# Kernel tuning notes

Measured on AMD Instinct MI355X. Metric: run time of the kernel, lower is better.

## Reference

```python
import jax, jax.numpy as jnp
import numpy as np

PREFIX = 20000
LEAF = 50000
NONLEAF = 50000
NUMD = 8 * NONLEAF  # 400000 fine-depth nodes
C = 256


def setup_inputs() -> dict:
    key = jax.random.key(0)
    k1, k2 = jax.random.split(key)
    n_rows = PREFIX + LEAF + NUMD
    x = jax.random.normal(k1, (n_rows, C), dtype=jnp.float32)
    # xavier-uniform-like init for Downsample weights (C_out, C_in, 8)
    limit = float(np.sqrt(6.0 / (C + C * 8)))
    weights = jax.random.uniform(k2, (C, C, 8), dtype=jnp.float32,
                                 minval=-limit, maxval=limit)
    # children at depth-1: alternate leaf (-1) / non-leaf (+1) -> exactly LEAF leaves
    children = jnp.where(jnp.arange(LEAF + NONLEAF) % 2 == 0, -1, 1).astype(jnp.int32)
    return {"x": x, "weights": weights, "children": children,
            "numd": NUMD, "leaf_num": LEAF}


def reference(x, weights, children, numd, leaf_num):
    c = x.shape[1]
    # Downsample: groups of 8 fine nodes -> one coarse node.
    # torch: x.view(-1, 8*C) @ weights.flatten(1).t()
    outd = x[-numd:].reshape(-1, 8 * c) @ weights.reshape(c, 8 * c).T  # [numd/8, C]

    leaf_mask = children < 0                      # [nnum_prev]
    lm = leaf_mask.astype(jnp.int32)
    rank_leaf = jnp.cumsum(lm) - lm               # rank among leaf positions
    nlm = 1 - lm
    rank_nonleaf = jnp.cumsum(nlm) - nlm          # rank among non-leaf positions
    # out[leaf_mask] = x[-leaf_num-numd:-numd]; out[~leaf_mask] = outd
    idx = jnp.where(leaf_mask, rank_leaf, leaf_num + rank_nonleaf)
    x_leaf = x[-(leaf_num + numd):-numd]          # [leaf_num, C]
    combined = jnp.concatenate([x_leaf, outd], axis=0)
    merged = combined[idx]                        # [nnum_prev, C]

    prefix = x.shape[0] - leaf_num - numd
    return jnp.concatenate([x[:prefix], merged], axis=0)
```

## Files before the change

### kernel.cpp

```cpp
#include <hip/hip_runtime.h>
#include <hip/hip_bf16.h>

#define PREFIX_N 20000
#define LEAF_N   50000
#define NONLEAF_N 50000
#define CH_N     (LEAF_N + NONLEAF_N)
#define CCOL     256
#define GK       2048
#define GM       NONLEAF_N
#define OUT_ROWS (PREFIX_N + CH_N)
#define NKT      (GK / 32)

typedef float  f32x4v __attribute__((ext_vector_type(4)));
typedef __bf16 bf16x8 __attribute__((ext_vector_type(8)));
typedef short  s16x8  __attribute__((ext_vector_type(8)));

static __device__ __forceinline__ unsigned pk2(float a, float b) {
  __hip_bfloat16 ha = __float2bfloat16(a);
  __hip_bfloat16 hb = __float2bfloat16(b);
  unsigned short sa = __builtin_bit_cast(unsigned short, ha);
  unsigned short sb = __builtin_bit_cast(unsigned short, hb);
  return (unsigned)sa | ((unsigned)sb << 16);
}
static __device__ __forceinline__ uint4 pack8(const float4& x, const float4& y) {
  uint4 r;
  r.x = pk2(x.x, x.y); r.y = pk2(x.z, x.w);
  r.z = pk2(y.x, y.y); r.w = pk2(y.z, y.w);
  return r;
}

__global__ __launch_bounds__(256) void count_leaves(const int* __restrict__ ch,
                                                    int n, int* __restrict__ cnt) {
  int gi = blockIdx.x * 256 + threadIdx.x;
  int lm = (gi < n && ch[gi] < 0) ? 1 : 0;
  unsigned long long mask = __ballot(lm);
  __shared__ int wsum[4];
  int lane = threadIdx.x & 63, w = threadIdx.x >> 6;
  if (lane == 0) wsum[w] = __popcll(mask);
  __syncthreads();
  if (threadIdx.x == 0) cnt[blockIdx.x] = wsum[0] + wsum[1] + wsum[2] + wsum[3];
}

__global__ __launch_bounds__(512) void scan_blocks(const int* __restrict__ cnt,
                                                   int* __restrict__ boff, int nb) {
  __shared__ int s[512];
  int t = threadIdx.x;
  int v = (t < nb) ? cnt[t] : 0;
  s[t] = v;
  __syncthreads();
  for (int d = 1; d < 512; d <<= 1) {
    int add = (t >= d) ? s[t - d] : 0;
    __syncthreads();
    s[t] += add;
    __syncthreads();
  }
  if (t < nb) boff[t] = s[t] - v;
}

__global__ __launch_bounds__(256) void rank_kernel(const int* __restrict__ ch,
                                                   const int* __restrict__ boff, int n,
                                                   int* __restrict__ idx,
                                                   int* __restrict__ rowof) {
  int gi = blockIdx.x * 256 + threadIdx.x;
  int lane = threadIdx.x & 63, w = threadIdx.x >> 6;
  int lm = (gi < n && ch[gi] < 0) ? 1 : 0;
  unsigned long long mask = __ballot(lm);
  int lrank = __popcll(mask & ((1ull << lane) - 1ull));
  __shared__ int wcnt[4];
  if (lane == 63) wcnt[w] = lrank + lm;
  __syncthreads();
  int woff = 0;
  for (int i = 0; i < w; ++i) woff += wcnt[i];
  if (gi < n) {
    int rl = boff[blockIdx.x] + woff + lrank;
    if (lm) {
      idx[gi] = rl;
    } else {
      int rn = gi - rl;
      idx[gi] = LEAF_N + rn;
      rowof[rn] = gi;
    }
  }
}

__global__ __launch_bounds__(256) void copy_rows(const float* __restrict__ x,
                                                 const int* __restrict__ idx,
                                                 float* __restrict__ out) {
  int row = blockIdx.x * 4 + (threadIdx.x >> 6);
  if (row >= OUT_ROWS) return;
  int lane = threadIdx.x & 63;
  const float* src;
  if (row < PREFIX_N) {
    src = x + (size_t)row * CCOL;
  } else {
    int id = idx[row - PREFIX_N];
    if (id >= LEAF_N) return;
    src = x + (size_t)(PREFIX_N + id) * CCOL;
  }
  float4 v = ((const float4*)src)[lane];
  ((float4*)(out + (size_t)row * CCOL))[lane] = v;
}

__global__ __launch_bounds__(512, 2) void gemm_kernel(const float* __restrict__ A,
                                                      const float* __restrict__ W,
                                                      const int* __restrict__ rowof,
                                                      float* __restrict__ out) {
  __shared__ unsigned short Alds[128][40];
  __shared__ unsigned short Blds[256][40];
  __shared__ int tgt[128];

  const int tid  = threadIdx.x;
  const int lane = tid & 63;
  const int w    = tid >> 6;
  const int wm   = w >> 2;
  const int wn   = w & 3;
  const int tile_m = blockIdx.x;

  if (tid < 128) {
    int m = tile_m * 128 + tid;
    tgt[tid] = (m < GM) ? (PREFIX_N + rowof[m]) : -1;
  }

  const int ar = tid >> 2;
  const int ac = (tid & 3) * 8;
  const int br = tid >> 1;
  const int bc = (tid & 1) * 16;

  int agr = tile_m * 128 + ar;
  if (agr >= GM) agr = GM - 1;
  const float* aptr = A + (size_t)agr * GK + ac;
  const float* bptr = W + (size_t)br  * GK + bc;

  f32x4v acc[4][4] = {};

  float4 fa0, fa1, fb0, fb1, fb2, fb3;
  fa0 = ((const float4*)aptr)[0]; fa1 = ((const float4*)aptr)[1];
  fb0 = ((const float4*)bptr)[0]; fb1 = ((const float4*)bptr)[1];
  fb2 = ((const float4*)bptr)[2]; fb3 = ((const float4*)bptr)[3];
  uint4 aS  = pack8(fa0, fa1);
  uint4 bS0 = pack8(fb0, fb1);
  uint4 bS1 = pack8(fb2, fb3);

  const int lr = lane & 15, lq = lane >> 4;

  for (int kt = 0; kt < NKT; ++kt) {
    __syncthreads();
    *(uint4*)&Alds[ar][ac]     = aS;
    *(uint4*)&Blds[br][bc]     = bS0;
    *(uint4*)&Blds[br][bc + 8] = bS1;
    __syncthreads();

    if (kt + 1 < NKT) {
      const float* ap = aptr + (kt + 1) * 32;
      fa0 = ((const float4*)ap)[0]; fa1 = ((const float4*)ap)[1];
      const float* bp = bptr + (kt + 1) * 32;
      fb0 = ((const float4*)bp)[0]; fb1 = ((const float4*)bp)[1];
      fb2 = ((const float4*)bp)[2]; fb3 = ((const float4*)bp)[3];
    }

    s16x8 af[4], bf[4];
#pragma unroll
    for (int fm = 0; fm < 4; ++fm)
      af[fm] = *(const s16x8*)&Alds[wm * 64 + fm * 16 + lr][lq * 8];
#pragma unroll
    for (int fn = 0; fn < 4; ++fn)
      bf[fn] = *(const s16x8*)&Blds[wn * 64 + fn * 16 + lr][lq * 8];
#pragma unroll
    for (int fm = 0; fm < 4; ++fm)
#pragma unroll
      for (int fn = 0; fn < 4; ++fn)
        acc[fm][fn] = __builtin_amdgcn_mfma_f32_16x16x32_bf16(
            __builtin_bit_cast(bf16x8, af[fm]),
            __builtin_bit_cast(bf16x8, bf[fn]),
            acc[fm][fn], 0, 0, 0);

    if (kt + 1 < NKT) {
      aS  = pack8(fa0, fa1);
      bS0 = pack8(fb0, fb1);
      bS1 = pack8(fb2, fb3);
    }
  }

#pragma unroll
  for (int fm = 0; fm < 4; ++fm) {
    int mlb = wm * 64 + fm * 16 + lq * 4;
    int t0 = tgt[mlb + 0], t1 = tgt[mlb + 1], t2 = tgt[mlb + 2], t3 = tgt[mlb + 3];
#pragma unroll
    for (int fn = 0; fn < 4; ++fn) {
      int col = wn * 64 + fn * 16 + lr;
      if (t0 >= 0) out[(size_t)t0 * CCOL + col] = acc[fm][fn][0];
      if (t1 >= 0) out[(size_t)t1 * CCOL + col] = acc[fm][fn][1];
      if (t2 >= 0) out[(size_t)t2 * CCOL + col] = acc[fm][fn][2];
      if (t3 >= 0) out[(size_t)t3 * CCOL + col] = acc[fm][fn][3];
    }
  }
}

extern "C" void kernel_launch(void* const* d_in, const int* in_sizes, int n_in,
                              void* d_out, int out_size, void* d_ws, size_t ws_size,
                              hipStream_t stream) {
  const float* x        = (const float*)d_in[0];
  const float* wts      = (const float*)d_in[1];
  const int*   children = (const int*)d_in[2];
  float*       out      = (float*)d_out;

  int* wsp   = (int*)d_ws;
  int* cnt   = wsp;
  int* boff  = wsp + 512;
  int* idx   = wsp + 1024;
  int* rowof = wsp + 1024 + CH_N;

  const int nb = (CH_N + 255) / 256;

  count_leaves<<<nb, 256, 0, stream>>>(children, CH_N, cnt);
  scan_blocks<<<1, 512, 0, stream>>>(cnt, boff, nb);
  rank_kernel<<<nb, 256, 0, stream>>>(children, boff, CH_N, idx, rowof);

  copy_rows<<<(OUT_ROWS + 3) / 4, 256, 0, stream>>>(x, idx, out);

  const float* A = x + (size_t)(PREFIX_N + LEAF_N) * CCOL;
  gemm_kernel<<<(GM + 127) / 128, 512, 0, stream>>>(A, wts, rowof, out);
}
```

Baseline: 204.1 us.

## Pre-convert weights to bf16 and double-buffer GEMM tiles with direct global-to-LDS loads

A new kernel converts the weights to bf16 once per call into workspace. The GEMM then streams B tiles straight into LDS with global_load_lds, using XOR-swizzled, double-buffered LDS tiles for both operands. A tiles are prefetched two k-steps ahead in registers. This removes per-block fp32-to-bf16 conversion of W and overlaps loads with MFMA work, at the cost of an extra launch, more LDS, hand-placed waitcnt/barrier sequencing and dropping the occupancy hint of 2.

```diff
diff --git a/kernel.cpp b/kernel.cpp
--- a/kernel.cpp
+++ b/kernel.cpp
@@ -27,6 +27,18 @@
   r.x = pk2(x.x, x.y); r.y = pk2(x.z, x.w);
   r.z = pk2(y.x, y.y); r.w = pk2(y.z, y.w);
   return r;
+}
+
+#define GLDS16(g, l) __builtin_amdgcn_global_load_lds(                      \
+    (const __attribute__((address_space(1))) void*)(g),                     \
+    (__attribute__((address_space(3))) void*)(l), 16, 0, 0)
+
+__global__ __launch_bounds__(256) void wcvt(const float* __restrict__ W,
+                                            unsigned short* __restrict__ Wb) {
+  int i = blockIdx.x * 256 + threadIdx.x;
+  float4 a = ((const float4*)W)[i * 2];
+  float4 b = ((const float4*)W)[i * 2 + 1];
+  *(uint4*)&Wb[i * 8] = pack8(a, b);
 }
 
 __global__ __launch_bounds__(256) void count_leaves(const int* __restrict__ ch,
@@ -101,12 +113,12 @@
   ((float4*)(out + (size_t)row * CCOL))[lane] = v;
 }
 
-__global__ __launch_bounds__(512, 2) void gemm_kernel(const float* __restrict__ A,
-                                                      const float* __restrict__ W,
-                                                      const int* __restrict__ rowof,
-                                                      float* __restrict__ out) {
-  __shared__ unsigned short Alds[128][40];
-  __shared__ unsigned short Blds[256][40];
+__global__ __launch_bounds__(512) void gemm_kernel(const float* __restrict__ A,
+                                                   const unsigned short* __restrict__ Wb,
+                                                   const int* __restrict__ rowof,
+                                                   float* __restrict__ out) {
+  __shared__ unsigned short Abuf[2][128 * 32];
+  __shared__ unsigned short Bbuf[2][256 * 32];
   __shared__ int tgt[128];
 
   const int tid  = threadIdx.x;
@@ -114,6 +126,7 @@
   const int w    = tid >> 6;
   const int wm   = w >> 2;
   const int wn   = w & 3;
+  const int lr   = lane & 15, lq = lane >> 4;
   const int tile_m = blockIdx.x;
 
   if (tid < 128) {
@@ -123,63 +136,77 @@
 
   const int ar = tid >> 2;
   const int ac = (tid & 3) * 8;
-  const int br = tid >> 1;
-  const int bc = (tid & 1) * 16;
-
   int agr = tile_m * 128 + ar;
   if (agr >= GM) agr = GM - 1;
   const float* aptr = A + (size_t)agr * GK + ac;
-  const float* bptr = W + (size_t)br  * GK + bc;
+  const int awidx = ar * 32 + (((tid & 3) ^ ((ar >> 1) & 3)) << 3);
+
+  const int brow0 = (w << 4) + (lane >> 2);
+  const int bch0  = (lane & 3) ^ ((brow0 >> 1) & 3);
+  const int brow1 = brow0 + 128;
+  const int bch1  = (lane & 3) ^ ((brow1 >> 1) & 3);
+  const char* bsrc0 = (const char*)Wb + (size_t)brow0 * (GK * 2) + (bch0 << 4);
+  const char* bsrc1 = (const char*)Wb + (size_t)brow1 * (GK * 2) + (bch1 << 4);
+  char* bd0_0 = (char*)&Bbuf[0][0] + tid * 16;
+  char* bd1_0 = bd0_0 + 8192;
+  char* bd0_1 = (char*)&Bbuf[1][0] + tid * 16;
+  char* bd1_1 = bd0_1 + 8192;
+
+  int aidx[4], bidx[4];
+#pragma unroll
+  for (int fm = 0; fm < 4; ++fm) {
+    int row = wm * 64 + fm * 16 + lr;
+    aidx[fm] = row * 32 + ((lq ^ ((row >> 1) & 3)) << 3);
+  }
+#pragma unroll
+  for (int fn = 0; fn < 4; ++fn) {
+    int row = wn * 64 + fn * 16 + lr;
+    bidx[fn] = row * 32 + ((lq ^ ((row >> 1) & 3)) << 3);
+  }
 
   f32x4v acc[4][4] = {};
-
-  float4 fa0, fa1, fb0, fb1, fb2, fb3;
-  fa0 = ((const float4*)aptr)[0]; fa1 = ((const float4*)aptr)[1];
-  fb0 = ((const float4*)bptr)[0]; fb1 = ((const float4*)bptr)[1];
-  fb2 = ((const float4*)bptr)[2]; fb3 = ((const float4*)bptr)[3];
-  uint4 aS  = pack8(fa0, fa1);
-  uint4 bS0 = pack8(fb0, fb1);
-  uint4 bS1 = pack8(fb2, fb3);
-
-  const int lr = lane & 15, lq = lane >> 4;
-
-  for (int kt = 0; kt < NKT; ++kt) {
-    __syncthreads();
-    *(uint4*)&Alds[ar][ac]     = aS;
-    *(uint4*)&Blds[br][bc]     = bS0;
-    *(uint4*)&Blds[br][bc + 8] = bS1;
-    __syncthreads();
-
-    if (kt + 1 < NKT) {
-      const float* ap = aptr + (kt + 1) * 32;
-      fa0 = ((const float4*)ap)[0]; fa1 = ((const float4*)ap)[1];
-      const float* bp = bptr + (kt + 1) * 32;
-      fb0 = ((const float4*)bp)[0]; fb1 = ((const float4*)bp)[1];
-      fb2 = ((const float4*)bp)[2]; fb3 = ((const float4*)bp)[3];
-    }
-
-    s16x8 af[4], bf[4];
-#pragma unroll
-    for (int fm = 0; fm < 4; ++fm)
-      af[fm] = *(const s16x8*)&Alds[wm * 64 + fm * 16 + lr][lq * 8];
-#pragma unroll
-    for (int fn = 0; fn < 4; ++fn)
-      bf[fn] = *(const s16x8*)&Blds[wn * 64 + fn * 16 + lr][lq * 8];
-#pragma unroll
-    for (int fm = 0; fm < 4; ++fm)
-#pragma unroll
-      for (int fn = 0; fn < 4; ++fn)
-        acc[fm][fn] = __builtin_amdgcn_mfma_f32_16x16x32_bf16(
-            __builtin_bit_cast(bf16x8, af[fm]),
-            __builtin_bit_cast(bf16x8, bf[fn]),
-            acc[fm][fn], 0, 0, 0);
-
-    if (kt + 1 < NKT) {
-      aS  = pack8(fa0, fa1);
-      bS0 = pack8(fb0, fb1);
-      bS1 = pack8(fb2, fb3);
-    }
-  }
+  float4 rAa0, rAa1, rAb0, rAb1;
+
+  GLDS16(bsrc0, bd0_0); GLDS16(bsrc1, bd1_0);
+  rAa0 = ((const float4*)aptr)[0]; rAa1 = ((const float4*)aptr)[1];
+  GLDS16(bsrc0 + 64, bd0_1); GLDS16(bsrc1 + 64, bd1_1);
+  rAb0 = ((const float4*)(aptr + 32))[0]; rAb1 = ((const float4*)(aptr + 32))[1];
+  *(uint4*)&Abuf[0][awidx] = pack8(rAa0, rAa1);
+  asm volatile("s_waitcnt lgkmcnt(0)" ::: "memory");
+  __builtin_amdgcn_s_barrier();
+
+#define GBODY(n_, CUR, RAc0, RAc1, RAl0, RAl1, BD0, BD1)                     \
+  {                                                                          \
+    s16x8 af[4], bf[4];                                                      \
+    _Pragma("unroll") for (int fm = 0; fm < 4; ++fm)                         \
+        af[fm] = *(const s16x8*)&Abuf[CUR][aidx[fm]];                        \
+    _Pragma("unroll") for (int fn = 0; fn < 4; ++fn)                         \
+        bf[fn] = *(const s16x8*)&Bbuf[CUR][bidx[fn]];                        \
+    asm volatile("s_waitcnt lgkmcnt(0)" ::: "memory");                       \
+    __builtin_amdgcn_s_barrier();                                            \
+    if ((n_) + 1 < NKT)                                                      \
+      *(uint4*)&Abuf[CUR ^ 1][awidx] = pack8(RAc0, RAc1);                    \
+    if ((n_) + 2 < NKT) {                                                    \
+      GLDS16(bsrc0 + ((n_) + 2) * 64, BD0);                                  \
+      GLDS16(bsrc1 + ((n_) + 2) * 64, BD1);                                  \
+      RAl0 = ((const float4*)(aptr + ((n_) + 2) * 32))[0];                   \
+      RAl1 = ((const float4*)(aptr + ((n_) + 2) * 32))[1];                   \
+    }                                                                        \
+    _Pragma("unroll") for (int fm = 0; fm < 4; ++fm)                         \
+      _Pragma("unroll") for (int fn = 0; fn < 4; ++fn)                       \
+          acc[fm][fn] = __builtin_amdgcn_mfma_f32_16x16x32_bf16(             \
+              __builtin_bit_cast(bf16x8, af[fm]),                            \
+              __builtin_bit_cast(bf16x8, bf[fn]), acc[fm][fn], 0, 0, 0);     \
+    asm volatile("s_waitcnt lgkmcnt(0)" ::: "memory");                       \
+    __builtin_amdgcn_s_barrier();                                            \
+  }
+
+#pragma unroll 1
+  for (int n = 0; n < NKT; n += 2) {
+    GBODY(n,     0, rAb0, rAb1, rAa0, rAa1, bd0_0, bd1_0);
+    GBODY(n + 1, 1, rAa0, rAa1, rAb0, rAb1, bd0_1, bd1_1);
+  }
+#undef GBODY
 
 #pragma unroll
   for (int fm = 0; fm < 4; ++fm) {
@@ -209,9 +236,11 @@
   int* boff  = wsp + 512;
   int* idx   = wsp + 1024;
   int* rowof = wsp + 1024 + CH_N;
+  unsigned short* Wb = (unsigned short*)((char*)d_ws + (1 << 20));
 
   const int nb = (CH_N + 255) / 256;
 
+  wcvt<<<256, 256, 0, stream>>>(wts, Wb);
   count_leaves<<<nb, 256, 0, stream>>>(children, CH_N, cnt);
   scan_blocks<<<1, 512, 0, stream>>>(cnt, boff, nb);
   rank_kernel<<<nb, 256, 0, stream>>>(children, boff, CH_N, idx, rowof);
@@ -219,5 +248,5 @@
   copy_rows<<<(OUT_ROWS + 3) / 4, 256, 0, stream>>>(x, idx, out);
 
   const float* A = x + (size_t)(PREFIX_N + LEAF_N) * CCOL;
-  gemm_kernel<<<(GM + 127) / 128, 512, 0, stream>>>(A, wts, rowof, out);
-}
+  gemm_kernel<<<(GM + 127) / 128, 512, 0, stream>>>(A, Wb, rowof, out);
+}
```

Result: slower. 224.3 us (+9.9%).

## Pre-convert weights to bf16, fuse row copy into GEMM, stream B from global

Applied to the files above, without the earlier changes.

The weight matrix is converted to bf16 once in a prep kernel that also counts leaves. The GEMM now uses 64-row tiles, 256 threads and double-buffered A in LDS with a K-step of 64, and B fragments are read directly from the bf16 global copy, leaving LDS for A only. The leaf and prefix row copy is folded into the same launch as extra blocks using a scatter map (leafof), which removes a kernel launch and the idx array. The intent is to cut weight conversion work, launch count and LDS traffic. In exchange, B reloads from global/L2 per tile become heavier and there are more GEMM blocks.

```diff
diff --git a/kernel.cpp b/kernel.cpp
--- a/kernel.cpp
+++ b/kernel.cpp
@@ -9,7 +9,12 @@
 #define GK       2048
 #define GM       NONLEAF_N
 #define OUT_ROWS (PREFIX_N + CH_N)
-#define NKT      (GK / 32)
+#define BM       64
+#define BKT      64
+#define NKT      (GK / BKT)
+#define TILES    ((GM + BM - 1) / BM)
+#define COPYROWS (PREFIX_N + LEAF_N)
+#define COPYBLK  ((COPYROWS + 3) / 4)
 
 typedef float  f32x4v __attribute__((ext_vector_type(4)));
 typedef __bf16 bf16x8 __attribute__((ext_vector_type(8)));
@@ -29,16 +34,26 @@
   return r;
 }
 
-__global__ __launch_bounds__(256) void count_leaves(const int* __restrict__ ch,
-                                                    int n, int* __restrict__ cnt) {
-  int gi = blockIdx.x * 256 + threadIdx.x;
-  int lm = (gi < n && ch[gi] < 0) ? 1 : 0;
-  unsigned long long mask = __ballot(lm);
-  __shared__ int wsum[4];
-  int lane = threadIdx.x & 63, w = threadIdx.x >> 6;
-  if (lane == 0) wsum[w] = __popcll(mask);
-  __syncthreads();
-  if (threadIdx.x == 0) cnt[blockIdx.x] = wsum[0] + wsum[1] + wsum[2] + wsum[3];
+__global__ __launch_bounds__(256) void prep_kernel(const float* __restrict__ W,
+                                                   unsigned short* __restrict__ Wb,
+                                                   const int* __restrict__ ch,
+                                                   int* __restrict__ cnt) {
+  if (blockIdx.x < 256) {
+    int i = blockIdx.x * 256 + threadIdx.x;
+    float4 a = ((const float4*)W)[i * 2];
+    float4 b = ((const float4*)W)[i * 2 + 1];
+    *(uint4*)&Wb[i * 8] = pack8(a, b);
+  } else {
+    int blk = blockIdx.x - 256;
+    int gi = blk * 256 + threadIdx.x;
+    int lm = (gi < CH_N && ch[gi] < 0) ? 1 : 0;
+    unsigned long long mask = __ballot(lm);
+    __shared__ int wsum[4];
+    int lane = threadIdx.x & 63, w = threadIdx.x >> 6;
+    if (lane == 0) wsum[w] = __popcll(mask);
+    __syncthreads();
+    if (threadIdx.x == 0) cnt[blk] = wsum[0] + wsum[1] + wsum[2] + wsum[3];
+  }
 }
 
 __global__ __launch_bounds__(512) void scan_blocks(const int* __restrict__ cnt,
@@ -59,8 +74,8 @@
 
 __global__ __launch_bounds__(256) void rank_kernel(const int* __restrict__ ch,
                                                    const int* __restrict__ boff, int n,
-                                                   int* __restrict__ idx,
-                                                   int* __restrict__ rowof) {
+                                                   int* __restrict__ rowof,
+                                                   int* __restrict__ leafof) {
   int gi = blockIdx.x * 256 + threadIdx.x;
   int lane = threadIdx.x & 63, w = threadIdx.x >> 6;
   int lm = (gi < n && ch[gi] < 0) ? 1 : 0;
@@ -73,117 +88,108 @@
   for (int i = 0; i < w; ++i) woff += wcnt[i];
   if (gi < n) {
     int rl = boff[blockIdx.x] + woff + lrank;
-    if (lm) {
-      idx[gi] = rl;
-    } else {
-      int rn = gi - rl;
-      idx[gi] = LEAF_N + rn;
-      rowof[rn] = gi;
-    }
-  }
-}
-
-__global__ __launch_bounds__(256) void copy_rows(const float* __restrict__ x,
-                                                 const int* __restrict__ idx,
-                                                 float* __restrict__ out) {
-  int row = blockIdx.x * 4 + (threadIdx.x >> 6);
-  if (row >= OUT_ROWS) return;
-  int lane = threadIdx.x & 63;
-  const float* src;
-  if (row < PREFIX_N) {
-    src = x + (size_t)row * CCOL;
-  } else {
-    int id = idx[row - PREFIX_N];
-    if (id >= LEAF_N) return;
-    src = x + (size_t)(PREFIX_N + id) * CCOL;
-  }
-  float4 v = ((const float4*)src)[lane];
-  ((float4*)(out + (size_t)row * CCOL))[lane] = v;
-}
-
-__global__ __launch_bounds__(512, 2) void gemm_kernel(const float* __restrict__ A,
-                                                      const float* __restrict__ W,
+    if (lm) leafof[rl] = gi;
+    else    rowof[gi - rl] = gi;
+  }
+}
+
+__global__ __launch_bounds__(256, 3) void main_kernel(const float* __restrict__ x,
+                                                      const float* __restrict__ A,
+                                                      const unsigned short* __restrict__ Wb,
                                                       const int* __restrict__ rowof,
+                                                      const int* __restrict__ leafof,
                                                       float* __restrict__ out) {
-  __shared__ unsigned short Alds[128][40];
-  __shared__ unsigned short Blds[256][40];
-  __shared__ int tgt[128];
+  __shared__ unsigned short Al[2][BM * 72];
+  __shared__ int tgt[BM];
 
   const int tid  = threadIdx.x;
   const int lane = tid & 63;
-  const int w    = tid >> 6;
-  const int wm   = w >> 2;
-  const int wn   = w & 3;
-  const int tile_m = blockIdx.x;
-
-  if (tid < 128) {
-    int m = tile_m * 128 + tid;
+
+  if (blockIdx.x >= TILES) {
+    int j = (blockIdx.x - TILES) * 4 + (tid >> 6);
+    if (j >= COPYROWS) return;
+    const float* src;
+    float* dst;
+    if (j < PREFIX_N) {
+      src = x + (size_t)j * CCOL;
+      dst = out + (size_t)j * CCOL;
+    } else {
+      int r = j - PREFIX_N;
+      src = x + (size_t)(PREFIX_N + r) * CCOL;
+      dst = out + (size_t)(PREFIX_N + leafof[r]) * CCOL;
+    }
+    ((float4*)dst)[lane] = ((const float4*)src)[lane];
+    return;
+  }
+
+  const int wn = tid >> 6;
+  const int lr = lane & 15, lq = lane >> 4;
+  const int tile = blockIdx.x;
+
+  if (tid < BM) {
+    int m = tile * BM + tid;
     tgt[tid] = (m < GM) ? (PREFIX_N + rowof[m]) : -1;
   }
 
   const int ar = tid >> 2;
-  const int ac = (tid & 3) * 8;
-  const int br = tid >> 1;
-  const int bc = (tid & 1) * 16;
-
-  int agr = tile_m * 128 + ar;
+  const int ac = (tid & 3) * 16;
+  int agr = tile * BM + ar;
   if (agr >= GM) agr = GM - 1;
   const float* aptr = A + (size_t)agr * GK + ac;
-  const float* bptr = W + (size_t)br  * GK + bc;
+  const int aw = ar * 72 + ac;
+
+  const unsigned short* bbase[4];
+#pragma unroll
+  for (int fn = 0; fn < 4; ++fn)
+    bbase[fn] = Wb + (size_t)(wn * 64 + fn * 16 + lr) * GK + lq * 8;
+
+  int aidx[4];
+#pragma unroll
+  for (int fm = 0; fm < 4; ++fm)
+    aidx[fm] = (fm * 16 + lr) * 72 + lq * 8;
 
   f32x4v acc[4][4] = {};
-
-  float4 fa0, fa1, fb0, fb1, fb2, fb3;
-  fa0 = ((const float4*)aptr)[0]; fa1 = ((const float4*)aptr)[1];
-  fb0 = ((const float4*)bptr)[0]; fb1 = ((const float4*)bptr)[1];
-  fb2 = ((const float4*)bptr)[2]; fb3 = ((const float4*)bptr)[3];
-  uint4 aS  = pack8(fa0, fa1);
-  uint4 bS0 = pack8(fb0, fb1);
-  uint4 bS1 = pack8(fb2, fb3);
-
-  const int lr = lane & 15, lq = lane >> 4;
-
+  float4 r0, r1, r2, r3;
+  r0 = ((const float4*)aptr)[0]; r1 = ((const float4*)aptr)[1];
+  r2 = ((const float4*)aptr)[2]; r3 = ((const float4*)aptr)[3];
+
+  int cur = 0;
+#pragma unroll 1
   for (int kt = 0; kt < NKT; ++kt) {
-    __syncthreads();
-    *(uint4*)&Alds[ar][ac]     = aS;
-    *(uint4*)&Blds[br][bc]     = bS0;
-    *(uint4*)&Blds[br][bc + 8] = bS1;
+    *(uint4*)&Al[cur][aw]     = pack8(r0, r1);
+    *(uint4*)&Al[cur][aw + 8] = pack8(r2, r3);
     __syncthreads();
 
     if (kt + 1 < NKT) {
-      const float* ap = aptr + (kt + 1) * 32;
-      fa0 = ((const float4*)ap)[0]; fa1 = ((const float4*)ap)[1];
-      const float* bp = bptr + (kt + 1) * 32;
-      fb0 = ((const float4*)bp)[0]; fb1 = ((const float4*)bp)[1];
-      fb2 = ((const float4*)bp)[2]; fb3 = ((const float4*)bp)[3];
-    }
-
-    s16x8 af[4], bf[4];
-#pragma unroll
-    for (int fm = 0; fm < 4; ++fm)
-      af[fm] = *(const s16x8*)&Alds[wm * 64 + fm * 16 + lr][lq * 8];
-#pragma unroll
-    for (int fn = 0; fn < 4; ++fn)
-      bf[fn] = *(const s16x8*)&Blds[wn * 64 + fn * 16 + lr][lq * 8];
-#pragma unroll
-    for (int fm = 0; fm < 4; ++fm)
+      const float* p = aptr + (kt + 1) * BKT;
+      r0 = ((const float4*)p)[0]; r1 = ((const float4*)p)[1];
+      r2 = ((const float4*)p)[2]; r3 = ((const float4*)p)[3];
+    }
+
+#pragma unroll
+    for (int ks = 0; ks < 2; ++ks) {
+      s16x8 af[4], bf[4];
+#pragma unroll
+      for (int fm = 0; fm < 4; ++fm)
+        af[fm] = *(const s16x8*)&Al[cur][aidx[fm] + ks * 32];
 #pragma unroll
       for (int fn = 0; fn < 4; ++fn)
-        acc[fm][fn] = __builtin_amdgcn_mfma_f32_16x16x32_bf16(
-            __builtin_bit_cast(bf16x8, af[fm]),
-            __builtin_bit_cast(bf16x8, bf[fn]),
-            acc[fm][fn], 0, 0, 0);
-
-    if (kt + 1 < NKT) {
-      aS  = pack8(fa0, fa1);
-      bS0 = pack8(fb0, fb1);
-      bS1 = pack8(fb2, fb3);
-    }
+        bf[fn] = *(const s16x8*)&bbase[fn][kt * BKT + ks * 32];
+#pragma unroll
+      for (int fm = 0; fm < 4; ++fm)
+#pragma unroll
+        for (int fn = 0; fn < 4; ++fn)
+          acc[fm][fn] = __builtin_amdgcn_mfma_f32_16x16x32_bf16(
+              __builtin_bit_cast(bf16x8, af[fm]),
+              __builtin_bit_cast(bf16x8, bf[fn]),
+              acc[fm][fn], 0, 0, 0);
+    }
+    cur ^= 1;
   }
 
 #pragma unroll
   for (int fm = 0; fm < 4; ++fm) {
-    int mlb = wm * 64 + fm * 16 + lq * 4;
+    int mlb = fm * 16 + lq * 4;
     int t0 = tgt[mlb + 0], t1 = tgt[mlb + 1], t2 = tgt[mlb + 2], t3 = tgt[mlb + 3];
 #pragma unroll
     for (int fn = 0; fn < 4; ++fn) {
@@ -204,20 +210,19 @@
   const int*   children = (const int*)d_in[2];
   float*       out      = (float*)d_out;
 
-  int* wsp   = (int*)d_ws;
-  int* cnt   = wsp;
-  int* boff  = wsp + 512;
-  int* idx   = wsp + 1024;
-  int* rowof = wsp + 1024 + CH_N;
+  int* wsp    = (int*)d_ws;
+  int* cnt    = wsp;
+  int* boff   = wsp + 512;
+  int* rowof  = wsp + 1024;
+  int* leafof = wsp + 1024 + GM;
+  unsigned short* Wb = (unsigned short*)((char*)d_ws + (1 << 20));
 
   const int nb = (CH_N + 255) / 256;
 
-  count_leaves<<<nb, 256, 0, stream>>>(children, CH_N, cnt);
+  prep_kernel<<<256 + nb, 256, 0, stream>>>(wts, Wb, children, cnt);
   scan_blocks<<<1, 512, 0, stream>>>(cnt, boff, nb);
-  rank_kernel<<<nb, 256, 0, stream>>>(children, boff, CH_N, idx, rowof);
-
-  copy_rows<<<(OUT_ROWS + 3) / 4, 256, 0, stream>>>(x, idx, out);
+  rank_kernel<<<nb, 256, 0, stream>>>(children, boff, CH_N, rowof, leafof);
 
   const float* A = x + (size_t)(PREFIX_N + LEAF_N) * CCOL;
-  gemm_kernel<<<(GM + 127) / 128, 512, 0, stream>>>(A, wts, rowof, out);
-}
+  main_kernel<<<TILES + COPYBLK, 256, 0, stream>>>(x, A, Wb, rowof, leafof, out);
+}
```

After: 217.0 us. +6.3%, slower.
